# Optimization experiments

Hardware: AMD Instinct MI355X
Metric: run time of the kernel (lower is better)

The kernel has to match this reference:

```python
import jax, jax.numpy as jnp
import numpy as np

B, S, D = 2, 2048, 1024
H, DK = 16, 64


def setup_inputs() -> dict:
    key = jax.random.key(0)
    ks = jax.random.split(key, 10)
    scale = D ** -0.5
    x = jax.random.normal(ks[0], (B, S, D), dtype=jnp.float32)
    mask = jax.random.randint(ks[1], (B, S), 0, 2) > 0  # True = masked positions
    Wq = jax.random.normal(ks[2], (D, H * DK), dtype=jnp.float32) * scale
    Wk = jax.random.normal(ks[3], (D, H * DK), dtype=jnp.float32) * scale
    Wv = jax.random.normal(ks[4], (D, H * DK), dtype=jnp.float32) * scale
    Wo = jax.random.normal(ks[5], (H * DK, D), dtype=jnp.float32) * scale
    bq = jnp.zeros((H * DK,), jnp.float32)
    bk = jnp.zeros((H * DK,), jnp.float32)
    bv = jnp.zeros((H * DK,), jnp.float32)
    bo = jnp.zeros((D,), jnp.float32)
    return {"x": x, "mask": mask, "Wq": Wq, "bq": bq, "Wk": Wk, "bk": bk,
            "Wv": Wv, "bv": bv, "Wo": Wo, "bo": bo}


def reference(x, mask, Wq, bq, Wk, bk, Wv, bv, Wo, bo):
    b, s, _ = x.shape
    # Linear + activation (dropout is identity at eval)
    q = jax.nn.relu(x @ Wq + bq).reshape(b, s, H, DK)
    k = jax.nn.relu(x @ Wk + bk).reshape(b, s, H, DK)
    v = jax.nn.relu(x @ Wv + bv).reshape(b, s, H, DK)
    # scores: [B, H, Sq, Sk]
    attn = jnp.einsum("bqhd,bkhd->bhqk", q, k) * (DK ** -0.5)
    # NOTE: original uses masked_fill(mask, 1e-9) BEFORE softmax (not -inf)
    attn = jnp.where(mask[:, None, None, :], jnp.float32(1e-9), attn)
    attn = jax.nn.softmax(attn, axis=-1)
    out = jnp.einsum("bhqk,bkhd->bqhd", attn, v).reshape(b, s, H * DK)
    return jax.nn.relu(out @ Wo + bo)
```

## Files before the change

kernel.cpp:

```cpp
#include <hip/hip_runtime.h>
#include <stdint.h>

typedef __attribute__((ext_vector_type(8))) short short8;
typedef __attribute__((ext_vector_type(4))) short short4b;
typedef __attribute__((ext_vector_type(4))) float f32x4;
typedef __attribute__((ext_vector_type(4))) unsigned short ushort4_t;

#define MFMA16(a, b, c) __builtin_amdgcn_mfma_f32_16x16x32_bf16((a), (b), (c), 0, 0, 0)

#if defined(__HIP_DEVICE_COMPILE__)
  #if __has_builtin(__builtin_amdgcn_mfma_f32_16x16x16bf16_1k)
    #define MFMA16K16(a, b, c) __builtin_amdgcn_mfma_f32_16x16x16bf16_1k((a), (b), (c), 0, 0, 0)
  #else
    #define MFMA16K16(a, b, c) __builtin_amdgcn_mfma_f32_16x16x16_bf16((a), (b), (c), 0, 0, 0)
  #endif
#else
  #define MFMA16K16(a, b, c) (c)
#endif

__device__ __forceinline__ float b2f(unsigned short u) {
    union { unsigned u; float f; } c; c.u = ((unsigned)u) << 16; return c.f;
}
__device__ __forceinline__ unsigned short f2b(float f) {
    union { float f; unsigned u; } c; c.f = f;
    unsigned r = c.u + 0x7FFF + ((c.u >> 16) & 1);
    return (unsigned short)(r >> 16);
}
__device__ __forceinline__ unsigned f_as_u(float f) {
    union { float f; unsigned u; } c; c.f = f; return c.u;
}

__device__ __forceinline__ void g2lds16(const unsigned short* g, unsigned lds_byte_off) {
    __builtin_amdgcn_global_load_lds(
        (const __attribute__((address_space(1))) void*)(uintptr_t)g,
        (__attribute__((address_space(3))) void*)(uintptr_t)lds_byte_off,
        16, 0, 0);
}

__global__ void detect_dtype(const unsigned short* __restrict__ x, int* __restrict__ flag) {
    __shared__ int cnt;
    if (threadIdx.x == 0) cnt = 0;
    __syncthreads();
    int insane = 0;
    #pragma unroll
    for (int j = 0; j < 4; ++j) {
        unsigned short u = x[threadIdx.x * 4 + j];
        int e = (u >> 7) & 0xFF;
        if ((e >= 1 && e <= 90) || e >= 165) insane++;
    }
    atomicAdd(&cnt, insane);
    __syncthreads();
    if (threadIdx.x == 0) *flag = (cnt > 128) ? 1 : 0;
}

__global__ __launch_bounds__(256) void convtrans_k(const void* __restrict__ s0, const void* __restrict__ s1,
                                                   const void* __restrict__ s2, const void* __restrict__ s3,
                                                   const void* __restrict__ b0, const void* __restrict__ b1,
                                                   const void* __restrict__ b2, const void* __restrict__ b3s,
                                                   const void* __restrict__ xsrc,
                                                   unsigned short* __restrict__ xdst,
                                                   unsigned short* __restrict__ dstBase,
                                                   unsigned short* __restrict__ dstB3,
                                                   unsigned short* __restrict__ dstBo,
                                                   const int* __restrict__ flag) {
    const int z = blockIdx.z;
    if (z >= 5) {
        if (!*flag) return;
        const int slice = z - 5;
        const size_t i0 = (size_t)slice * 524288 + (blockIdx.y * 16 + blockIdx.x) * 2048 + threadIdx.x * 8;
        const float* s = (const float*)xsrc;
        float4 f0 = *(const float4*)&s[i0];
        float4 f1 = *(const float4*)&s[i0 + 4];
        unsigned short* t = &xdst[i0];
        t[0] = f2b(f0.x); t[1] = f2b(f0.y); t[2] = f2b(f0.z); t[3] = f2b(f0.w);
        t[4] = f2b(f1.x); t[5] = f2b(f1.y); t[6] = f2b(f1.z); t[7] = f2b(f1.w);
        return;
    }
    if (z == 4) {
        if (blockIdx.y != 0 || blockIdx.x >= 4) return;
        const int w = blockIdx.x;
        const void* src = (w == 0) ? b0 : (w == 1) ? b1 : (w == 2) ? b2 : b3s;
        #pragma unroll
        for (int j = 0; j < 4; ++j) {
            const int i = threadIdx.x * 4 + j;
            unsigned short v = (*flag) ? f2b(((const float*)src)[i]) : ((const unsigned short*)src)[i];
            if (w < 3) dstB3[w * 1024 + i] = v;
            else dstBo[i] = v;
        }
        return;
    }
    __shared__ __align__(16) unsigned short tile[64 * 72];
    const void* src = (z == 0) ? s0 : (z == 1) ? s1 : (z == 2) ? s2 : s3;
    unsigned short* dst = dstBase + (size_t)z * 1024 * 1024;
    const int tid = threadIdx.x;
    const int r0 = blockIdx.y * 64, c0 = blockIdx.x * 64;
    const int rb = tid >> 3, c = (tid & 7) * 8;
    if (*flag) {
        const float* s = (const float*)src;
        #pragma unroll
        for (int it = 0; it < 2; ++it) {
            int rr = it * 32 + rb;
            float4 f0 = *(const float4*)&s[(size_t)(r0 + rr) * 1024 + c0 + c];
            float4 f1 = *(const float4*)&s[(size_t)(r0 + rr) * 1024 + c0 + c + 4];
            unsigned short* t = &tile[rr * 72 + c];
            t[0] = f2b(f0.x); t[1] = f2b(f0.y); t[2] = f2b(f0.z); t[3] = f2b(f0.w);
            t[4] = f2b(f1.x); t[5] = f2b(f1.y); t[6] = f2b(f1.z); t[7] = f2b(f1.w);
        }
    } else {
        const unsigned short* s = (const unsigned short*)src;
        #pragma unroll
        for (int it = 0; it < 2; ++it) {
            int rr = it * 32 + rb;
            *(short8*)&tile[rr * 72 + c] = *(const short8*)&s[(size_t)(r0 + rr) * 1024 + c0 + c];
        }
    }
    __syncthreads();
    #pragma unroll
    for (int it = 0; it < 2; ++it) {
        int n = it * 32 + rb, k8 = c;
        union { short8 s; unsigned short u[8]; } tmp;
        #pragma unroll
        for (int j = 0; j < 8; ++j) tmp.u[j] = tile[(k8 + j) * 72 + n];
        *(short8*)&dst[(size_t)(c0 + n) * 1024 + r0 + k8] = tmp.s;
    }
}

__global__ __launch_bounds__(256) void gemm_bias_relu(const unsigned short* __restrict__ A,
                                                      const void* __restrict__ Araw,
                                                      const unsigned short* __restrict__ BT,
                                                      const unsigned short* __restrict__ bias,
                                                      void* __restrict__ C,
                                                      unsigned short* __restrict__ VtG,
                                                      const int* __restrict__ flag,
                                                      int M, int N, int K, int mode) {
    __shared__ __align__(16) unsigned short As[128 * 32];
    __shared__ __align__(16) unsigned short Bs[128 * 32];
    const int tid = threadIdx.x;
    const int wave = tid >> 6, lane = tid & 63;
    const int quad = lane >> 4, l16 = lane & 15;
    const int wm = wave >> 1, wn = wave & 1;
    const int m0 = blockIdx.y * 128, n0 = blockIdx.x * 128;

    const unsigned short* Ause = (Araw != nullptr && *flag == 0) ? (const unsigned short*)Araw : A;

    f32x4 acc[4][4];
    #pragma unroll
    for (int i = 0; i < 4; i++)
        #pragma unroll
        for (int j = 0; j < 4; j++) acc[i][j] = (f32x4){0.f, 0.f, 0.f, 0.f};

    const int srow = wave * 32 + (lane >> 2);
    const int sc8  = (lane & 3) * 8;
    const unsigned short* gA0 = Ause + (size_t)(m0 + srow) * K + sc8;
    const unsigned short* gA1 = gA0 + (size_t)16 * K;
    const unsigned short* gB0 = BT + (size_t)(n0 + srow) * K + sc8;
    const unsigned short* gB1 = gB0 + (size_t)16 * K;
    const unsigned ldsA = (unsigned)(uintptr_t)&As[0] + wave * 2048;
    const unsigned ldsB = (unsigned)(uintptr_t)&Bs[0] + wave * 2048;

    for (int k0 = 0; k0 < K; k0 += 32) {
        __syncthreads();
        g2lds16(gA0 + k0, ldsA);
        g2lds16(gA1 + k0, ldsA + 1024);
        g2lds16(gB0 + k0, ldsB);
        g2lds16(gB1 + k0, ldsB + 1024);
        __syncthreads();
        short8 af[4], bf[4];
        #pragma unroll
        for (int i = 0; i < 4; i++) af[i] = *(const short8*)&As[(wm * 64 + i * 16 + l16) * 32 + quad * 8];
        #pragma unroll
        for (int j = 0; j < 4; j++) bf[j] = *(const short8*)&Bs[(wn * 64 + j * 16 + l16) * 32 + quad * 8];
        #pragma unroll
        for (int i = 0; i < 4; i++)
            #pragma unroll
            for (int j = 0; j < 4; j++)
                acc[i][j] = MFMA16(af[i], bf[j], acc[i][j]);
    }

    if (mode == 2 && n0 >= 2048) {
        #pragma unroll
        for (int j = 0; j < 4; j++) {
            const int col = n0 + wn * 64 + j * 16 + l16;
            const int h  = (col - 2048) >> 6;
            const int dk = (col - 2048) & 63;
            const float bj = b2f(bias[col]);
            #pragma unroll
            for (int i = 0; i < 4; i++) {
                const int rowb = m0 + wm * 64 + i * 16 + quad * 4;
                const int bb = rowb >> 11;
                const int s0 = rowb & 2047;
                ushort4_t w;
                #pragma unroll
                for (int r = 0; r < 4; r++) {
                    float v = acc[i][j][r] + bj;
                    v = v > 0.f ? v : 0.f;
                    w[r] = f2b(v);
                }
                *(ushort4_t*)&VtG[(size_t)((bb * 16 + h) * 64 + dk) * 2048 + s0] = w;
            }
        }
    } else {
        const int f32out = (mode == 1) && (*flag != 0);
        #pragma unroll
        for (int j = 0; j < 4; j++) {
            const int col = n0 + wn * 64 + j * 16 + l16;
            const float bj = b2f(bias[col]);
            #pragma unroll
            for (int i = 0; i < 4; i++) {
                const int rowb = m0 + wm * 64 + i * 16 + quad * 4;
                #pragma unroll
                for (int r = 0; r < 4; r++) {
                    float v = acc[i][j][r] + bj;
                    v = v > 0.f ? v : 0.f;
                    if (f32out) ((float*)C)[(size_t)(rowb + r) * N + col] = v;
                    else ((unsigned short*)C)[(size_t)(rowb + r) * N + col] = f2b(v);
                }
            }
        }
    }
}

__global__ __launch_bounds__(256) void attn_kernel(const unsigned short* __restrict__ qkv,
                                                   const unsigned short* __restrict__ VtG,
                                                   const int* __restrict__ mask,
                                                   unsigned short* __restrict__ out) {
    __shared__ __align__(16) unsigned short Ks[64 * 72];
    __shared__ __align__(16) unsigned short Vs[64 * 72];
    __shared__ __align__(16) float maskF[2048];

    const int qt = blockIdx.x, bh = blockIdx.y;
    const int b = bh >> 4, h = bh & 15;
    const int tid = threadIdx.x, wave = tid >> 6, lane = tid & 63;
    const int quad = lane >> 4, l16 = lane & 15;

    const float SCL = 0.125f * 1.44269504f;
    for (int i = tid; i < 2048; i += 256) maskF[i] = mask[b * 2048 + i] ? 0.f : SCL;

    const int qrowA = qt * 128 + wave * 16 + l16;
    const unsigned short* qpA = qkv + (size_t)(b * 2048 + qrowA) * 3072 + h * 64;
    const unsigned short* qpB = qpA + (size_t)64 * 3072;
    const short8 qa0 = *(const short8*)(qpA + quad * 8);
    const short8 qa1 = *(const short8*)(qpA + 32 + quad * 8);
    const short8 qb0 = *(const short8*)(qpB + quad * 8);
    const short8 qb1 = *(const short8*)(qpB + 32 + quad * 8);

    f32x4 oA[4], oB[4], sumA, sumB;
    #pragma unroll
    for (int n = 0; n < 4; n++) { oA[n] = (f32x4){0.f,0.f,0.f,0.f}; oB[n] = (f32x4){0.f,0.f,0.f,0.f}; }
    sumA = (f32x4){0.f,0.f,0.f,0.f};
    sumB = (f32x4){0.f,0.f,0.f,0.f};

    const short4b ones = { (short)0x3F80, (short)0x3F80, (short)0x3F80, (short)0x3F80 };

    const int srow = tid >> 2;
    const int scol = (tid & 3) * 16;
    const unsigned short* kg = qkv + (size_t)(b * 2048 + srow) * 3072 + 1024 + h * 64 + scol;
    const unsigned short* vg = VtG + (size_t)(bh * 64 + srow) * 2048 + scol;
    const size_t kstep = (size_t)64 * 3072;
    unsigned short* wK = &Ks[srow * 72 + scol];
    unsigned short* wV = &Vs[srow * 72 + scol];

    for (int kt = 0; kt < 32; ++kt) {
        __syncthreads();
        *(short8*)wK       = *(const short8*)(kg + kt * kstep);
        *(short8*)(wK + 8) = *(const short8*)(kg + kt * kstep + 8);
        *(short8*)wV       = *(const short8*)(vg + kt * 64);
        *(short8*)(wV + 8) = *(const short8*)(vg + kt * 64 + 8);
        __syncthreads();

        f32x4 sA[4], sB[4];
        #pragma unroll
        for (int t = 0; t < 4; ++t) {
            const short8 kb0 = *(const short8*)&Ks[(t * 16 + l16) * 72 + quad * 8];
            const short8 kb1 = *(const short8*)&Ks[(t * 16 + l16) * 72 + 32 + quad * 8];
            f32x4 z = (f32x4){0.f, 0.f, 0.f, 0.f};
            sA[t] = MFMA16(kb1, qa1, MFMA16(kb0, qa0, z));
            sB[t] = MFMA16(kb1, qb1, MFMA16(kb0, qb0, z));
        }

        short4b vb[4][4];
        #pragma unroll
        for (int t = 0; t < 4; ++t)
            #pragma unroll
            for (int n = 0; n < 4; ++n)
                vb[t][n] = *(const short4b*)&Vs[(n * 16 + l16) * 72 + t * 16 + quad * 4];

        #pragma unroll
        for (int t = 0; t < 4; ++t) {
            const f32x4 scl = *(const f32x4*)&maskF[kt * 64 + t * 16 + quad * 4];
            float pA[4], pB[4];
            #pragma unroll
            for (int r = 0; r < 4; ++r) {
                pA[r] = exp2f(sA[t][r] * scl[r]);
                pB[r] = exp2f(sB[t][r] * scl[r]);
            }
            union { unsigned u[2]; short4b s; } fa, fb;
            fa.u[0] = __builtin_amdgcn_perm(f_as_u(pA[1]), f_as_u(pA[0]), 0x07060302u);
            fa.u[1] = __builtin_amdgcn_perm(f_as_u(pA[3]), f_as_u(pA[2]), 0x07060302u);
            fb.u[0] = __builtin_amdgcn_perm(f_as_u(pB[1]), f_as_u(pB[0]), 0x07060302u);
            fb.u[1] = __builtin_amdgcn_perm(f_as_u(pB[3]), f_as_u(pB[2]), 0x07060302u);
            #pragma unroll
            for (int n = 0; n < 4; ++n) {
                oA[n] = MFMA16K16(fa.s, vb[t][n], oA[n]);
                oB[n] = MFMA16K16(fb.s, vb[t][n], oB[n]);
            }
            sumA = MFMA16K16(fa.s, ones, sumA);
            sumB = MFMA16K16(fb.s, ones, sumB);
        }
    }

    float invA[4], invB[4];
    #pragma unroll
    for (int r = 0; r < 4; ++r) { invA[r] = 1.0f / sumA[r]; invB[r] = 1.0f / sumB[r]; }
    #pragma unroll
    for (int n = 0; n < 4; n++)
        #pragma unroll
        for (int r = 0; r < 4; r++) {
            const int row = qt * 128 + wave * 16 + quad * 4 + r;
            out[(size_t)(b * 2048 + row) * 1024 + h * 64 + n * 16 + l16] = f2b(oA[n][r] * invA[r]);
            out[(size_t)(b * 2048 + row + 64) * 1024 + h * 64 + n * 16 + l16] = f2b(oB[n][r] * invB[r]);
        }
}

extern "C" void kernel_launch(void* const* d_in, const int* in_sizes, int n_in,
                              void* d_out, int out_size, void* d_ws, size_t ws_size,
                              hipStream_t stream) {
    const void* x  = d_in[0];
    const int*  mk = (const int*)d_in[1];
    const void* Wq = d_in[2]; const void* bq = d_in[3];
    const void* Wk = d_in[4]; const void* bk = d_in[5];
    const void* Wv = d_in[6]; const void* bv = d_in[7];
    const void* Wo = d_in[8]; const void* bo = d_in[9];

    char* wsb = (char*)d_ws;
    int* flag = (int*)wsb;
    unsigned short* W0 = (unsigned short*)(wsb + 64);

    const size_t M1 = 1024u * 1024u;
    const size_t M4 = 4096u * 1024u;
    unsigned short* xb  = W0;
    unsigned short* WT  = xb + M4;
    unsigned short* WoT = WT + 3 * M1;
    unsigned short* b3  = WoT + M1;
    unsigned short* bob = b3 + 4096;
    unsigned short* qkv = bob + 1024;
    unsigned short* VtG = qkv + (size_t)4096 * 3072;
    unsigned short* abf = xb;

    detect_dtype<<<1, 256, 0, stream>>>((const unsigned short*)x, flag);

    convtrans_k<<<dim3(16, 16, 13), 256, 0, stream>>>(Wq, Wk, Wv, Wo, bq, bk, bv, bo,
                                                      x, xb, WT, b3, bob, flag);

    gemm_bias_relu<<<dim3(24, 32), 256, 0, stream>>>(xb, x, WT, b3, qkv, VtG, flag, 4096, 3072, 1024, 2);
    attn_kernel<<<dim3(16, 32), 256, 0, stream>>>(qkv, VtG, mk, abf);
    gemm_bias_relu<<<dim3(8, 32), 256, 0, stream>>>(abf, nullptr, WoT, bob, d_out, VtG, flag, 4096, 1024, 1024, 1);
}
```

Before: 237.8 us.

## Fold softmax scale and key mask into QKV GEMM epilogue; use 64-row output GEMM

The QKV projection epilogue now pre-multiplies Q by the softmax scale (times log2 e) and zeroes K rows at masked positions. Attention can then call exp2 on raw scores, with no per-block mask table in LDS and no per-score multiply. A zeroed K gives a score of 0, which matches the reference's 1e-9 fill to within rounding. The output projection moves to a new 64x128-tile GEMM kernel, doubling the block count to fill the GPU better. The trade-off is extra bf16 rounding of the scaled Q and a less-reused smaller tile.

After: 250.0 us. 5.1% more time.

```diff
diff --git a/kernel.cpp b/kernel.cpp
--- a/kernel.cpp
+++ b/kernel.cpp
@@ -17,6 +17,8 @@
 #else
   #define MFMA16K16(a, b, c) (c)
 #endif
+
+#define SCL_F (0.125f * 1.44269504f)
 
 __device__ __forceinline__ float b2f(unsigned short u) {
     union { unsigned u; float f; } c; c.u = ((unsigned)u) << 16; return c.f;
@@ -131,6 +133,7 @@
                                                       const unsigned short* __restrict__ bias,
                                                       void* __restrict__ C,
                                                       unsigned short* __restrict__ VtG,
+                                                      const int* __restrict__ mask,
                                                       const int* __restrict__ flag,
                                                       int M, int N, int K, int mode) {
     __shared__ __align__(16) unsigned short As[128 * 32];
@@ -199,6 +202,29 @@
                 *(ushort4_t*)&VtG[(size_t)((bb * 16 + h) * 64 + dk) * 2048 + s0] = w;
             }
         }
+    } else if (mode == 2) {
+        const int isQ = (n0 < 1024);
+        #pragma unroll
+        for (int j = 0; j < 4; j++) {
+            const int col = n0 + wn * 64 + j * 16 + l16;
+            const float bj = b2f(bias[col]);
+            #pragma unroll
+            for (int i = 0; i < 4; i++) {
+                const int rowb = m0 + wm * 64 + i * 16 + quad * 4;
+                #pragma unroll
+                for (int r = 0; r < 4; r++) {
+                    float v = acc[i][j][r] + bj;
+                    v = v > 0.f ? v : 0.f;
+                    if (isQ) {
+                        v *= SCL_F;
+                    } else {
+                        const int row = rowb + r;
+                        if (mask[(row >> 11) * 2048 + (row & 2047)]) v = 0.f;
+                    }
+                    ((unsigned short*)C)[(size_t)(rowb + r) * N + col] = f2b(v);
+                }
+            }
+        }
     } else {
         const int f32out = (mode == 1) && (*flag != 0);
         #pragma unroll
@@ -220,21 +246,81 @@
     }
 }
 
+__global__ __launch_bounds__(256) void gemm_bias_relu_64(const unsigned short* __restrict__ A,
+                                                         const unsigned short* __restrict__ BT,
+                                                         const unsigned short* __restrict__ bias,
+                                                         void* __restrict__ C,
+                                                         const int* __restrict__ flag,
+                                                         int M, int N, int K) {
+    __shared__ __align__(16) unsigned short As[64 * 32];
+    __shared__ __align__(16) unsigned short Bs[128 * 32];
+    const int tid = threadIdx.x;
+    const int wave = tid >> 6, lane = tid & 63;
+    const int quad = lane >> 4, l16 = lane & 15;
+    const int wm = wave >> 1, wn = wave & 1;
+    const int m0 = blockIdx.y * 64, n0 = blockIdx.x * 128;
+
+    f32x4 acc[2][4];
+    #pragma unroll
+    for (int i = 0; i < 2; i++)
+        #pragma unroll
+        for (int j = 0; j < 4; j++) acc[i][j] = (f32x4){0.f, 0.f, 0.f, 0.f};
+
+    const int sr16 = lane >> 2;
+    const int sc8  = (lane & 3) * 8;
+    const unsigned short* gA0 = A  + (size_t)(m0 + wave * 16 + sr16) * K + sc8;
+    const unsigned short* gB0 = BT + (size_t)(n0 + wave * 32 + sr16) * K + sc8;
+    const unsigned short* gB1 = gB0 + (size_t)16 * K;
+    const unsigned ldsA = (unsigned)(uintptr_t)&As[0] + wave * 1024;
+    const unsigned ldsB = (unsigned)(uintptr_t)&Bs[0] + wave * 2048;
+
+    for (int k0 = 0; k0 < K; k0 += 32) {
+        __syncthreads();
+        g2lds16(gA0 + k0, ldsA);
+        g2lds16(gB0 + k0, ldsB);
+        g2lds16(gB1 + k0, ldsB + 1024);
+        __syncthreads();
+        short8 af[2], bf[4];
+        #pragma unroll
+        for (int i = 0; i < 2; i++) af[i] = *(const short8*)&As[(wm * 32 + i * 16 + l16) * 32 + quad * 8];
+        #pragma unroll
+        for (int j = 0; j < 4; j++) bf[j] = *(const short8*)&Bs[(wn * 64 + j * 16 + l16) * 32 + quad * 8];
+        #pragma unroll
+        for (int i = 0; i < 2; i++)
+            #pragma unroll
+            for (int j = 0; j < 4; j++)
+                acc[i][j] = MFMA16(af[i], bf[j], acc[i][j]);
+    }
+
+    const int f32out = (*flag != 0);
+    #pragma unroll
+    for (int j = 0; j < 4; j++) {
+        const int col = n0 + wn * 64 + j * 16 + l16;
+        const float bj = b2f(bias[col]);
+        #pragma unroll
+        for (int i = 0; i < 2; i++) {
+            const int rowb = m0 + wm * 32 + i * 16 + quad * 4;
+            #pragma unroll
+            for (int r = 0; r < 4; r++) {
+                float v = acc[i][j][r] + bj;
+                v = v > 0.f ? v : 0.f;
+                if (f32out) ((float*)C)[(size_t)(rowb + r) * N + col] = v;
+                else ((unsigned short*)C)[(size_t)(rowb + r) * N + col] = f2b(v);
+            }
+        }
+    }
+}
+
 __global__ __launch_bounds__(256) void attn_kernel(const unsigned short* __restrict__ qkv,
                                                    const unsigned short* __restrict__ VtG,
-                                                   const int* __restrict__ mask,
                                                    unsigned short* __restrict__ out) {
     __shared__ __align__(16) unsigned short Ks[64 * 72];
     __shared__ __align__(16) unsigned short Vs[64 * 72];
-    __shared__ __align__(16) float maskF[2048];
 
     const int qt = blockIdx.x, bh = blockIdx.y;
     const int b = bh >> 4, h = bh & 15;
     const int tid = threadIdx.x, wave = tid >> 6, lane = tid & 63;
     const int quad = lane >> 4, l16 = lane & 15;
-
-    const float SCL = 0.125f * 1.44269504f;
-    for (int i = tid; i < 2048; i += 256) maskF[i] = mask[b * 2048 + i] ? 0.f : SCL;
 
     const int qrowA = qt * 128 + wave * 16 + l16;
     const unsigned short* qpA = qkv + (size_t)(b * 2048 + qrowA) * 3072 + h * 64;
@@ -287,12 +373,11 @@
 
         #pragma unroll
         for (int t = 0; t < 4; ++t) {
-            const f32x4 scl = *(const f32x4*)&maskF[kt * 64 + t * 16 + quad * 4];
             float pA[4], pB[4];
             #pragma unroll
             for (int r = 0; r < 4; ++r) {
-                pA[r] = exp2f(sA[t][r] * scl[r]);
-                pB[r] = exp2f(sB[t][r] * scl[r]);
+                pA[r] = exp2f(sA[t][r]);
+                pB[r] = exp2f(sB[t][r]);
             }
             union { unsigned u[2]; short4b s; } fa, fb;
             fa.u[0] = __builtin_amdgcn_perm(f_as_u(pA[1]), f_as_u(pA[0]), 0x07060302u);
@@ -352,7 +437,9 @@
     convtrans_k<<<dim3(16, 16, 13), 256, 0, stream>>>(Wq, Wk, Wv, Wo, bq, bk, bv, bo,
                                                       x, xb, WT, b3, bob, flag);
 
-    gemm_bias_relu<<<dim3(24, 32), 256, 0, stream>>>(xb, x, WT, b3, qkv, VtG, flag, 4096, 3072, 1024, 2);
-    attn_kernel<<<dim3(16, 32), 256, 0, stream>>>(qkv, VtG, mk, abf);
-    gemm_bias_relu<<<dim3(8, 32), 256, 0, stream>>>(abf, nullptr, WoT, bob, d_out, VtG, flag, 4096, 1024, 1024, 1);
-}
+    gemm_bias_relu<<<dim3(24, 32), 256, 0, stream>>>(xb, x, WT, b3, qkv, VtG, mk, flag,
+                                                     4096, 3072, 1024, 2);
+    attn_kernel<<<dim3(16, 32), 256, 0, stream>>>(qkv, VtG, abf);
+    gemm_bias_relu_64<<<dim3(8, 64), 256, 0, stream>>>(abf, WoT, bob, d_out, flag,
+                                                       4096, 1024, 1024);
+}
```
